# Performance work log

Hardware: AMD Instinct MI355X
Metric: run time of the kernel (lower is better)

Reference implementation:

```python
import jax, jax.numpy as jnp
import numpy as np

HEADS = 8
OUT_PER_HEAD = 9
NEG_SLOPE = 0.2  # PyG GATConv default


def setup_inputs() -> dict:
    key = jax.random.key(0)
    k1, k2, k3, k4, k5, k6 = jax.random.split(key, 6)
    N, F_in, E = 100000, 12, 1600000
    x = jax.random.normal(k1, (N, F_in), dtype=jnp.float32)
    edge_index = jax.random.randint(k2, (2, E), 0, N, dtype=jnp.int64)
    # GATConv params: lin weight [F_in, H*C], attention vectors a_src/a_dst [H, C], bias [C] (concat=False)
    s = 1.0 / np.sqrt(F_in)
    W = jax.random.uniform(k3, (F_in, HEADS * OUT_PER_HEAD), minval=-s, maxval=s, dtype=jnp.float32)
    a_src = jax.random.uniform(k4, (HEADS, OUT_PER_HEAD), minval=-s, maxval=s, dtype=jnp.float32)
    a_dst = jax.random.uniform(k5, (HEADS, OUT_PER_HEAD), minval=-s, maxval=s, dtype=jnp.float32)
    bias = jnp.zeros((OUT_PER_HEAD,), dtype=jnp.float32)
    return {"x": x, "edge_index": edge_index, "W": W, "a_src": a_src, "a_dst": a_dst, "bias": bias}


def reference(x, edge_index, W, a_src, a_dst, bias):
    N = x.shape[0]
    # add self-loops (PyG GATConv default add_self_loops=True)
    loops = jnp.arange(N, dtype=edge_index.dtype)
    src = jnp.concatenate([edge_index[0], loops])
    dst = jnp.concatenate([edge_index[1], loops])
    # per-head linear transform: [N, H, C]
    h = (x @ W).reshape(N, HEADS, OUT_PER_HEAD)
    # node-level attention halves: [N, H]
    al_src = jnp.einsum('nhc,hc->nh', h, a_src)
    al_dst = jnp.einsum('nhc,hc->nh', h, a_dst)
    # edge-wise logits [E, H]
    e = jax.nn.leaky_relu(al_src[src] + al_dst[dst], NEG_SLOPE)
    # segment softmax over incoming edges of each destination node
    m = jax.ops.segment_max(e, dst, num_segments=N)  # [N, H]
    ex = jnp.exp(e - m[dst])
    denom = jax.ops.segment_sum(ex, dst, num_segments=N)  # [N, H]
    alpha = ex / (denom[dst] + jnp.float32(1e-16))
    # weighted scatter-aggregate: [N, H, C]
    out = jax.ops.segment_sum(alpha[:, :, None] * h[src], dst, num_segments=N)
    # concat=False -> mean over heads, then bias
    out = out.mean(axis=1) + bias
    # dropout is identity in eval; final log_softmax over feature dim
    return jax.nn.log_softmax(out, axis=1)
```

## Files before the change

kernel.cpp:

```cpp
#include <hip/hip_runtime.h>
#include <math.h>

#define NHEADS 8
#define NC 9
#define NHC 72
#define FIN 12
#define WAVES_PER_BLOCK 4
#define ROWW 48
#define ALS_OFF 36
#define MAXBUK 512
#define TILE 4096

__device__ __forceinline__ float lrelu(float v) { return v > 0.f ? v : 0.2f * v; }

__device__ __forceinline__ unsigned pack_bf16(float a, float b) {
    unsigned ua = __float_as_uint(a); ua += 0x7fffu + ((ua >> 16) & 1u);
    unsigned ub = __float_as_uint(b); ub += 0x7fffu + ((ub >> 16) & 1u);
    return (ua >> 16) | (ub & 0xffff0000u);
}

__global__ void __launch_bounds__(256) k_transform(
    const float* __restrict__ x, const float* __restrict__ W,
    const float* __restrict__ a_src, const float* __restrict__ a_dst,
    unsigned* __restrict__ hrow, float* __restrict__ al_d,
    const int* __restrict__ dst, int* __restrict__ bucket_count,
    int N, int E, int nbuk)
{
    __shared__ float sW[FIN * NHC];
    __shared__ float sas[NHC];
    __shared__ float sad[NHC];
    __shared__ int bcnt[MAXBUK];
    int tid = threadIdx.x;
    for (int i = tid; i < FIN * NHC; i += blockDim.x) sW[i] = W[i];
    if (tid < NHC) { sas[tid] = a_src[tid]; sad[tid] = a_dst[tid]; }
    for (int i = tid; i < nbuk; i += blockDim.x) bcnt[i] = 0;
    __syncthreads();
    int n = blockIdx.x * blockDim.x + tid;
    if (n < N) {
        float xv[FIN];
        const float4* xp = reinterpret_cast<const float4*>(x + (size_t)n * FIN);
        float4 q0 = xp[0], q1 = xp[1], q2 = xp[2];
        xv[0] = q0.x; xv[1] = q0.y; xv[2] = q0.z; xv[3] = q0.w;
        xv[4] = q1.x; xv[5] = q1.y; xv[6] = q1.z; xv[7] = q1.w;
        xv[8] = q2.x; xv[9] = q2.y; xv[10] = q2.z; xv[11] = q2.w;

        float acc[NHC];
        #pragma unroll
        for (int j = 0; j < NHC; ++j) acc[j] = 0.f;
        #pragma unroll
        for (int k = 0; k < FIN; ++k) {
            float xk = xv[k];
            #pragma unroll
            for (int j = 0; j < NHC; ++j) acc[j] = fmaf(xk, sW[k * NHC + j], acc[j]);
        }

        unsigned* rp = hrow + (size_t)n * ROWW;
        #pragma unroll
        for (int l = 0; l < NHC / 2; ++l)
            rp[l] = pack_bf16(acc[2 * l], acc[2 * l + 1]);

        float* rf = reinterpret_cast<float*>(rp);
        #pragma unroll
        for (int hh = 0; hh < NHEADS; ++hh) {
            float ss = 0.f, dd = 0.f;
            #pragma unroll
            for (int c = 0; c < NC; ++c) {
                ss = fmaf(acc[hh * NC + c], sas[hh * NC + c], ss);
                dd = fmaf(acc[hh * NC + c], sad[hh * NC + c], dd);
            }
            rf[ALS_OFF + hh] = ss;
            al_d[(size_t)n * NHEADS + hh] = dd;
        }
    }
    int stride = gridDim.x * blockDim.x;
    for (int i = blockIdx.x * blockDim.x + tid; i < E; i += stride)
        atomicAdd(&bcnt[dst[i] >> 8], 1);
    __syncthreads();
    for (int i = tid; i < nbuk; i += blockDim.x)
        if (bcnt[i]) atomicAdd(&bucket_count[i], bcnt[i]);
}

__global__ void __launch_bounds__(512) k_bscan(
    const int* __restrict__ bucket_count, int* __restrict__ bucket_base,
    int* __restrict__ gcur, int* __restrict__ rowptr, int nbuk, int N, int E)
{
    __shared__ int s[512];
    int t = threadIdx.x;
    int v = (t < nbuk) ? bucket_count[t] : 0;
    s[t] = v;
    __syncthreads();
    for (int off = 1; off < 512; off <<= 1) {
        int u = (t >= off) ? s[t - off] : 0;
        __syncthreads();
        s[t] += u;
        __syncthreads();
    }
    if (t < nbuk) {
        int ex = s[t] - v;
        bucket_base[t] = ex;
        gcur[t] = ex;
    }
    if (t == 0) { bucket_base[nbuk] = E; rowptr[N] = E; }
}

__global__ void __launch_bounds__(256) k_bucketA(
    const int* __restrict__ src, const int* __restrict__ dst,
    int* __restrict__ gcur, unsigned* __restrict__ bpair, int E, int nbuk)
{
    __shared__ int cnt[MAXBUK];
    __shared__ int sbase[MAXBUK];
    int t = threadIdx.x;
    for (int i = t; i < nbuk; i += 256) cnt[i] = 0;
    __syncthreads();
    int base0 = blockIdx.x * TILE;
    int rk[16], bk[16];
    unsigned pk[16];
    #pragma unroll
    for (int j = 0; j < 16; ++j) {
        int i = base0 + j * 256 + t;
        if (i < E) {
            int d = dst[i];
            int sg = src[i];
            bk[j] = d >> 8;
            pk[j] = (unsigned)sg | ((unsigned)(d & 255) << 24);
            rk[j] = atomicAdd(&cnt[bk[j]], 1);
        } else bk[j] = -1;
    }
    __syncthreads();
    for (int b = t; b < nbuk; b += 256)
        if (cnt[b]) sbase[b] = atomicAdd(&gcur[b], cnt[b]);
    __syncthreads();
    #pragma unroll
    for (int j = 0; j < 16; ++j)
        if (bk[j] >= 0) bpair[sbase[bk[j]] + rk[j]] = pk[j];
}

__global__ void __launch_bounds__(256) k_bucketB(
    const unsigned* __restrict__ bpair, const int* __restrict__ bucket_base,
    int* __restrict__ rowptr, int* __restrict__ sorted_src, int N)
{
    __shared__ int cnt[256];
    __shared__ int sc[256];
    int b = blockIdx.x;
    int t = threadIdx.x;
    int lo = bucket_base[b], hi = bucket_base[b + 1];
    cnt[t] = 0;
    __syncthreads();
    for (int i = lo + t; i < hi; i += 256)
        atomicAdd(&cnt[bpair[i] >> 24], 1);
    __syncthreads();
    int v = cnt[t];
    sc[t] = v;
    __syncthreads();
    for (int off = 1; off < 256; off <<= 1) {
        int u = (t >= off) ? sc[t - off] : 0;
        __syncthreads();
        sc[t] += u;
        __syncthreads();
    }
    int excl = sc[t] - v;
    int node = (b << 8) + t;
    if (node < N) rowptr[node] = lo + excl;
    __syncthreads();
    cnt[t] = lo + excl;
    __syncthreads();
    for (int i = lo + t; i < hi; i += 256) {
        unsigned w = bpair[i];
        int pos = atomicAdd(&cnt[w >> 24], 1);
        sorted_src[pos] = (int)(w & 0xFFFFFFu);
    }
}

__global__ void __launch_bounds__(256) k_gat(
    const int* __restrict__ rowptr, const int* __restrict__ sorted_src,
    const unsigned* __restrict__ hrow, const float* __restrict__ al_d,
    const float* __restrict__ bias, float* __restrict__ out, int N)
{
    __shared__ int   s_off[WAVES_PER_BLOCK][64];
    __shared__ float s_ex[WAVES_PER_BLOCK][64][9];
    __shared__ float s_den[WAVES_PER_BLOCK][8];
    __shared__ float s_out[WAVES_PER_BLOCK][NHC];
    __shared__ float s_v[WAVES_PER_BLOCK][NC];

    int wid  = threadIdx.x >> 6;
    int lane = threadIdx.x & 63;
    int n = blockIdx.x * WAVES_PER_BLOCK + wid;
    if (n >= N) return;

    int base  = rowptr[n];
    int total = rowptr[n + 1] - base + 1;

    int g  = lane >> 3;
    int hh = lane & 7;
    float ald_h = al_d[(size_t)n * NHEADS + hh];

    bool act36 = lane < NHC / 2;
    int widx4 = act36 ? lane * 4 : 0;
    int c0 = 2 * lane, c1 = 2 * lane + 1;
    int ha = act36 ? c0 / NC : 0;
    int hb = act36 ? c1 / NC : 0;
    float accA = 0.f, accB = 0.f;
    float den_part = 0.f;

    const char* hbase = reinterpret_cast<const char*>(hrow);
    int als_boff = (ALS_OFF + hh) * 4;

    for (int cb = 0; cb < total; cb += 64) {
        int rem = total - cb;
        int clen = rem < 64 ? rem : 64;
        int clenR = (clen + 3) & ~3;

        int j = cb + lane;
        int s = n;
        if (j < total - 1) s = sorted_src[base + j];
        s_off[wid][lane] = s * (ROWW * 4);

        for (int k = 0; k * 8 < clenR; ++k) {
            int lj = k * 8 + g;
            int off = s_off[wid][lj];
            float als = *reinterpret_cast<const float*>(hbase + off + als_boff);
            float ex = 0.f;
            if (cb + lj < total) ex = __expf(lrelu(als + ald_h));
            s_ex[wid][lj][hh] = ex;
            den_part += ex;
        }

        for (int e = 0; e < clenR; e += 4) {
            #pragma unroll
            for (int p = 0; p < 4; ++p) {
                int ee = e + p;
                int off = s_off[wid][ee];
                unsigned w = *reinterpret_cast<const unsigned*>(hbase + off + widx4);
                float fa = __uint_as_float(w << 16);
                float fb = __uint_as_float(w & 0xffff0000u);
                accA = fmaf(s_ex[wid][ee][ha], fa, accA);
                accB = fmaf(s_ex[wid][ee][hb], fb, accB);
            }
        }
    }

    den_part += __shfl_xor(den_part, 8, 64);
    den_part += __shfl_xor(den_part, 16, 64);
    den_part += __shfl_xor(den_part, 32, 64);
    if (lane < 8) s_den[wid][lane] = den_part;

    if (act36) {
        float ia = 1.f / (s_den[wid][ha] + 1e-16f);
        float ib = 1.f / (s_den[wid][hb] + 1e-16f);
        s_out[wid][c0] = accA * ia;
        s_out[wid][c1] = accB * ib;
    }

    if (lane < NC) {
        float v = 0.f;
        #pragma unroll
        for (int h = 0; h < NHEADS; ++h) v += s_out[wid][h * NC + lane];
        v = v * (1.f / NHEADS) + bias[lane];
        s_v[wid][lane] = v;
        float mx = -INFINITY;
        #pragma unroll
        for (int c = 0; c < NC; ++c) mx = fmaxf(mx, s_v[wid][c]);
        float sum = 0.f;
        #pragma unroll
        for (int c = 0; c < NC; ++c) sum += __expf(s_v[wid][c] - mx);
        float lse = mx + __logf(sum);
        out[(size_t)n * NC + lane] = s_v[wid][lane] - lse;
    }
}

extern "C" void kernel_launch(void* const* d_in, const int* in_sizes, int n_in,
                              void* d_out, int out_size, void* d_ws, size_t ws_size,
                              hipStream_t stream)
{
    const float* x     = (const float*)d_in[0];
    const int*   ei    = (const int*)d_in[1];
    const float* W     = (const float*)d_in[2];
    const float* a_src = (const float*)d_in[3];
    const float* a_dst = (const float*)d_in[4];
    const float* bias  = (const float*)d_in[5];

    int N = in_sizes[0] / FIN;
    int E = in_sizes[1] / 2;
    const int* src = ei;
    const int* dst = ei + E;
    int nbuk = (N + 255) >> 8;

    char* ws = (char*)d_ws;
    unsigned* hrow = (unsigned*)ws;     ws += (size_t)N * ROWW * sizeof(unsigned);
    float* al_d = (float*)ws;           ws += (size_t)N * NHEADS * sizeof(float);
    int* rowptr = (int*)ws;             ws += (size_t)(N + 1) * sizeof(int);
    int* bucket_count = (int*)ws;       ws += (size_t)(MAXBUK + 1) * sizeof(int);
    int* bucket_base  = (int*)ws;       ws += (size_t)(MAXBUK + 1) * sizeof(int);
    int* gcur = (int*)ws;               ws += (size_t)MAXBUK * sizeof(int);
    unsigned* bpair = (unsigned*)ws;    ws += (size_t)E * sizeof(unsigned);
    int* sorted_src = (int*)ws;         ws += (size_t)E * sizeof(int);

    hipMemsetAsync(bucket_count, 0, (size_t)(MAXBUK + 1) * sizeof(int), stream);

    int nb_n = (N + 255) / 256;
    int nb_a = (E + TILE - 1) / TILE;

    k_transform<<<nb_n, 256, 0, stream>>>(x, W, a_src, a_dst, hrow, al_d,
                                          dst, bucket_count, N, E, nbuk);
    k_bscan<<<1, 512, 0, stream>>>(bucket_count, bucket_base, gcur, rowptr,
                                   nbuk, N, E);
    k_bucketA<<<nb_a, 256, 0, stream>>>(src, dst, gcur, bpair, E, nbuk);
    k_bucketB<<<nbuk, 256, 0, stream>>>(bpair, bucket_base, rowptr, sorted_src, N);

    int nb_g = (N + WAVES_PER_BLOCK - 1) / WAVES_PER_BLOCK;
    k_gat<<<nb_g, 256, 0, stream>>>(rowptr, sorted_src, hrow, al_d, bias,
                                    (float*)d_out, N);
}
```

Measured before the change: 168.6 us.

## Gather 16-byte row chunks per lane, five edges per wave iteration

Reorganizes the aggregation in k_gat so each lane loads a uint4 chunk (8 bf16 features) of a neighbor row, and 12 lanes cover one padded row. Five edges are processed per wave step instead of one word per lane per edge. Attention source logits move to a separate contiguous array, and the row layout is padded to four 48-byte head-pair groups. Partial sums are combined with shared-memory atomics and normalized by precomputed reciprocal denominators. This cuts the number of gather instructions, at the cost of lanes 60-63 idling and some extra padded edge work.

```diff
diff --git a/kernel.cpp b/kernel.cpp
--- a/kernel.cpp
+++ b/kernel.cpp
@@ -5,11 +5,11 @@
 #define NC 9
 #define NHC 72
 #define FIN 12
-#define WAVES_PER_BLOCK 4
+#define WPB 4
 #define ROWW 48
-#define ALS_OFF 36
 #define MAXBUK 512
 #define TILE 4096
+#define EXW 10
 
 __device__ __forceinline__ float lrelu(float v) { return v > 0.f ? v : 0.2f * v; }
 
@@ -18,11 +18,13 @@
     unsigned ub = __float_as_uint(b); ub += 0x7fffu + ((ub >> 16) & 1u);
     return (ua >> 16) | (ub & 0xffff0000u);
 }
+__device__ __forceinline__ float blo(unsigned w) { return __uint_as_float(w << 16); }
+__device__ __forceinline__ float bhi(unsigned w) { return __uint_as_float(w & 0xffff0000u); }
 
 __global__ void __launch_bounds__(256) k_transform(
     const float* __restrict__ x, const float* __restrict__ W,
     const float* __restrict__ a_src, const float* __restrict__ a_dst,
-    unsigned* __restrict__ hrow, float* __restrict__ al_d,
+    unsigned* __restrict__ hrow, float* __restrict__ als_arr, float* __restrict__ al_d,
     const int* __restrict__ dst, int* __restrict__ bucket_count,
     int N, int E, int nbuk)
 {
@@ -54,12 +56,19 @@
             for (int j = 0; j < NHC; ++j) acc[j] = fmaf(xk, sW[k * NHC + j], acc[j]);
         }
 
-        unsigned* rp = hrow + (size_t)n * ROWW;
-        #pragma unroll
-        for (int l = 0; l < NHC / 2; ++l)
-            rp[l] = pack_bf16(acc[2 * l], acc[2 * l + 1]);
-
-        float* rf = reinterpret_cast<float*>(rp);
+        uint4* rp = reinterpret_cast<uint4*>(hrow + (size_t)n * ROWW);
+        #pragma unroll
+        for (int pp = 0; pp < 4; ++pp) {
+            const float* A = acc + pp * 18;
+            uint4 u0, u1, u2;
+            u0.x = pack_bf16(A[0],  A[1]);  u0.y = pack_bf16(A[2],  A[3]);
+            u0.z = pack_bf16(A[4],  A[5]);  u0.w = pack_bf16(A[6],  A[7]);
+            u1.x = pack_bf16(A[8],  A[9]);  u1.y = pack_bf16(A[10], A[11]);
+            u1.z = pack_bf16(A[12], A[13]); u1.w = pack_bf16(A[14], A[15]);
+            u2.x = pack_bf16(A[16], A[17]); u2.y = 0u; u2.z = 0u; u2.w = 0u;
+            rp[pp * 3 + 0] = u0; rp[pp * 3 + 1] = u1; rp[pp * 3 + 2] = u2;
+        }
+
         #pragma unroll
         for (int hh = 0; hh < NHEADS; ++hh) {
             float ss = 0.f, dd = 0.f;
@@ -68,7 +77,7 @@
                 ss = fmaf(acc[hh * NC + c], sas[hh * NC + c], ss);
                 dd = fmaf(acc[hh * NC + c], sad[hh * NC + c], dd);
             }
-            rf[ALS_OFF + hh] = ss;
+            als_arr[(size_t)n * NHEADS + hh] = ss;
             al_d[(size_t)n * NHEADS + hh] = dd;
         }
     }
@@ -173,18 +182,19 @@
 
 __global__ void __launch_bounds__(256) k_gat(
     const int* __restrict__ rowptr, const int* __restrict__ sorted_src,
-    const unsigned* __restrict__ hrow, const float* __restrict__ al_d,
-    const float* __restrict__ bias, float* __restrict__ out, int N)
-{
-    __shared__ int   s_off[WAVES_PER_BLOCK][64];
-    __shared__ float s_ex[WAVES_PER_BLOCK][64][9];
-    __shared__ float s_den[WAVES_PER_BLOCK][8];
-    __shared__ float s_out[WAVES_PER_BLOCK][NHC];
-    __shared__ float s_v[WAVES_PER_BLOCK][NC];
+    const unsigned* __restrict__ hrow, const float* __restrict__ als_arr,
+    const float* __restrict__ al_d, const float* __restrict__ bias,
+    float* __restrict__ out, int N)
+{
+    __shared__ int   s_src[WPB][66];
+    __shared__ float s_ex[WPB][65][EXW];
+    __shared__ float s_red[WPB][104];
+    __shared__ float s_den[WPB][8];
+    __shared__ float s_v[WPB][NC];
 
     int wid  = threadIdx.x >> 6;
     int lane = threadIdx.x & 63;
-    int n = blockIdx.x * WAVES_PER_BLOCK + wid;
+    int n = blockIdx.x * WPB + wid;
     if (n >= N) return;
 
     int base  = rowptr[n];
@@ -194,67 +204,86 @@
     int hh = lane & 7;
     float ald_h = al_d[(size_t)n * NHEADS + hh];
 
-    bool act36 = lane < NHC / 2;
-    int widx4 = act36 ? lane * 4 : 0;
-    int c0 = 2 * lane, c1 = 2 * lane + 1;
-    int ha = act36 ? c0 / NC : 0;
-    int hb = act36 ? c1 / NC : 0;
-    float accA = 0.f, accB = 0.f;
+    bool dummy = lane >= 60;
+    int e_loc = dummy ? 0 : lane / 12;
+    int unit  = dummy ? (lane - 60) : (lane - e_loc * 12);
+    int p = unit / 3;
+    int u = unit - p * 3;
+    int slot_base = dummy ? 96 : p * 24 + u * 8;
+    int row_boff = unit * 16;
+    int ex_off = 2 * p;
+    bool selF_B = (u == 2);
+    bool selR_A = (u == 0);
+
+    if (lane < EXW) s_ex[wid][64][lane] = 0.f;
+    s_red[wid][lane] = 0.f;
+    if (lane < 104 - 64) s_red[wid][64 + lane] = 0.f;
+
+    float acc[8];
+    #pragma unroll
+    for (int j = 0; j < 8; ++j) acc[j] = 0.f;
     float den_part = 0.f;
-
     const char* hbase = reinterpret_cast<const char*>(hrow);
-    int als_boff = (ALS_OFF + hh) * 4;
 
     for (int cb = 0; cb < total; cb += 64) {
         int rem = total - cb;
         int clen = rem < 64 ? rem : 64;
-        int clenR = (clen + 3) & ~3;
+        int padTo5 = ((clen + 4) / 5) * 5;
+        int cov    = padTo5 > 64 ? 64 : padTo5;
+        int clenR8 = (cov + 7) & ~7;
 
         int j = cb + lane;
         int s = n;
         if (j < total - 1) s = sorted_src[base + j];
-        s_off[wid][lane] = s * (ROWW * 4);
-
-        for (int k = 0; k * 8 < clenR; ++k) {
+        s_src[wid][lane] = s;
+        if (lane == 0) s_src[wid][64] = n;
+
+        for (int k = 0; k * 8 < clenR8; ++k) {
             int lj = k * 8 + g;
-            int off = s_off[wid][lj];
-            float als = *reinterpret_cast<const float*>(hbase + off + als_boff);
+            int sv = s_src[wid][lj];
+            float als = als_arr[(size_t)sv * NHEADS + hh];
             float ex = 0.f;
             if (cb + lj < total) ex = __expf(lrelu(als + ald_h));
             s_ex[wid][lj][hh] = ex;
             den_part += ex;
         }
 
-        for (int e = 0; e < clenR; e += 4) {
-            #pragma unroll
-            for (int p = 0; p < 4; ++p) {
-                int ee = e + p;
-                int off = s_off[wid][ee];
-                unsigned w = *reinterpret_cast<const unsigned*>(hbase + off + widx4);
-                float fa = __uint_as_float(w << 16);
-                float fb = __uint_as_float(w & 0xffff0000u);
-                accA = fmaf(s_ex[wid][ee][ha], fa, accA);
-                accB = fmaf(s_ex[wid][ee][hb], fb, accB);
-            }
+        for (int eb = 0; eb < padTo5; eb += 5) {
+            int ee = eb + e_loc;
+            int sv = s_src[wid][ee];
+            unsigned boff = (unsigned)sv * 192u + (unsigned)row_boff;
+            uint4 w4 = *reinterpret_cast<const uint4*>(hbase + boff);
+            float exA = s_ex[wid][ee][ex_off];
+            float exB = s_ex[wid][ee][ex_off + 1];
+            float exF = selF_B ? exB : exA;
+            float exR = selR_A ? exA : exB;
+            acc[0] = fmaf(exF, blo(w4.x), acc[0]);
+            acc[1] = fmaf(exR, bhi(w4.x), acc[1]);
+            acc[2] = fmaf(exR, blo(w4.y), acc[2]);
+            acc[3] = fmaf(exR, bhi(w4.y), acc[3]);
+            acc[4] = fmaf(exR, blo(w4.z), acc[4]);
+            acc[5] = fmaf(exR, bhi(w4.z), acc[5]);
+            acc[6] = fmaf(exR, blo(w4.w), acc[6]);
+            acc[7] = fmaf(exR, bhi(w4.w), acc[7]);
         }
     }
 
     den_part += __shfl_xor(den_part, 8, 64);
     den_part += __shfl_xor(den_part, 16, 64);
     den_part += __shfl_xor(den_part, 32, 64);
-    if (lane < 8) s_den[wid][lane] = den_part;
-
-    if (act36) {
-        float ia = 1.f / (s_den[wid][ha] + 1e-16f);
-        float ib = 1.f / (s_den[wid][hb] + 1e-16f);
-        s_out[wid][c0] = accA * ia;
-        s_out[wid][c1] = accB * ib;
-    }
+    if (lane < 8) s_den[wid][lane] = 1.f / (den_part + 1e-16f);
+
+    #pragma unroll
+    for (int jj = 0; jj < 8; ++jj)
+        atomicAdd(&s_red[wid][slot_base + jj], acc[jj]);
 
     if (lane < NC) {
         float v = 0.f;
         #pragma unroll
-        for (int h = 0; h < NHEADS; ++h) v += s_out[wid][h * NC + lane];
+        for (int h = 0; h < NHEADS; ++h) {
+            int pp = h >> 1, hi5 = h & 1;
+            v = fmaf(s_red[wid][pp * 24 + hi5 * 9 + lane], s_den[wid][h], v);
+        }
         v = v * (1.f / NHEADS) + bias[lane];
         s_v[wid][lane] = v;
         float mx = -INFINITY;
@@ -287,6 +316,7 @@
 
     char* ws = (char*)d_ws;
     unsigned* hrow = (unsigned*)ws;     ws += (size_t)N * ROWW * sizeof(unsigned);
+    float* als_arr = (float*)ws;        ws += (size_t)N * NHEADS * sizeof(float);
     float* al_d = (float*)ws;           ws += (size_t)N * NHEADS * sizeof(float);
     int* rowptr = (int*)ws;             ws += (size_t)(N + 1) * sizeof(int);
     int* bucket_count = (int*)ws;       ws += (size_t)(MAXBUK + 1) * sizeof(int);
@@ -300,14 +330,14 @@
     int nb_n = (N + 255) / 256;
     int nb_a = (E + TILE - 1) / TILE;
 
-    k_transform<<<nb_n, 256, 0, stream>>>(x, W, a_src, a_dst, hrow, al_d,
+    k_transform<<<nb_n, 256, 0, stream>>>(x, W, a_src, a_dst, hrow, als_arr, al_d,
                                           dst, bucket_count, N, E, nbuk);
     k_bscan<<<1, 512, 0, stream>>>(bucket_count, bucket_base, gcur, rowptr,
                                    nbuk, N, E);
     k_bucketA<<<nb_a, 256, 0, stream>>>(src, dst, gcur, bpair, E, nbuk);
     k_bucketB<<<nbuk, 256, 0, stream>>>(bpair, bucket_base, rowptr, sorted_src, N);
 
-    int nb_g = (N + WAVES_PER_BLOCK - 1) / WAVES_PER_BLOCK;
-    k_gat<<<nb_g, 256, 0, stream>>>(rowptr, sorted_src, hrow, al_d, bias,
+    int nb_g = (N + WPB - 1) / WPB;
+    k_gat<<<nb_g, 256, 0, stream>>>(rowptr, sorted_src, hrow, als_arr, al_d, bias,
                                     (float*)d_out, N);
 }
```

Result: slower. 378.6 us (+124.5%).
